# Kernel optimization log

Measured on AMD Instinct MI355X. Metric: run time of the kernel, lower is better.

## Reference

```python
import jax, jax.numpy as jnp
import numpy as np

PI = float(np.pi)


def _layernorm(x, g, b, eps=1e-5):
    mu = jnp.mean(x, axis=-1, keepdims=True)
    var = jnp.var(x, axis=-1, keepdims=True)
    return (x - mu) * jax.lax.rsqrt(var + eps) * g + b


def setup_inputs() -> dict:
    key = jax.random.key(0)
    B, L, D, P = 4, 2048, 256, 32
    ks = jax.random.split(key, 16)

    def lin_w(k, fi, fo):
        return (jax.random.normal(k, (fi, fo), dtype=jnp.float32) / np.sqrt(fi)).astype(jnp.float32)

    inp = {
        'x': jax.random.normal(ks[0], (B, L, D), dtype=jnp.float32),
        'pos_phases': jax.random.normal(ks[1], (L, P), dtype=jnp.float32) * PI,
        'w_mem1v': lin_w(ks[2], D, P), 'b_mem1v': jnp.zeros((P,), jnp.float32),
        'w_mem1o': lin_w(ks[3], P, D), 'b_mem1o': jnp.zeros((D,), jnp.float32),
        'w_off': lin_w(ks[4], D + P, P), 'b_off': jnp.zeros((P,), jnp.float32),
        'w_key': lin_w(ks[5], D, P), 'b_key': jnp.zeros((P,), jnp.float32),
        'w_val': lin_w(ks[6], D, D), 'b_val': jnp.zeros((D,), jnp.float32),
        'w_sk1': lin_w(ks[7], 2 * D, D), 'b_sk1': jnp.zeros((D,), jnp.float32),
        'w_sk2': lin_w(ks[8], D, P), 'b_sk2': jnp.zeros((P,), jnp.float32),
        'w_gate': lin_w(ks[9], D, 1), 'b_gate': jnp.zeros((1,), jnp.float32),
        'ln_g': jnp.ones((D,), jnp.float32), 'ln_b': jnp.zeros((D,), jnp.float32),
        'w_out': lin_w(ks[10], D, D), 'b_out': jnp.zeros((D,), jnp.float32),
    }
    return inp


def reference(x, pos_phases, w_mem1v, b_mem1v, w_mem1o, b_mem1o, w_off, b_off,
              w_key, b_key, w_val, b_val, w_sk1, b_sk1, w_sk2, b_sk2,
              w_gate, b_gate, ln_g, ln_b, w_out, b_out):
    B, L, D = x.shape
    P = pos_phases.shape[-1]

    pos_cos = jnp.cos(pos_phases)  # [L,P]
    pos_sin = jnp.sin(pos_phases)

    # Memory 1: flat [B,L,P] phasor cumulative memory
    v1 = x @ w_mem1v + b_mem1v                       # [B,L,P]
    mem1_cos = jnp.cumsum(pos_cos[None] * v1, axis=1)
    mem1_sin = jnp.cumsum(pos_sin[None] * v1, axis=1)

    offset_input = jnp.concatenate([x, jnp.broadcast_to(pos_phases[None], (B, L, P))], axis=-1)
    offset = jnp.tanh(offset_input @ w_off + b_off) * PI
    oc, os = jnp.cos(offset), jnp.sin(offset)
    query_cos = pos_cos[None] * oc - pos_sin[None] * os
    query_sin = pos_sin[None] * oc + pos_cos[None] * os
    pos_ret = (mem1_cos * query_cos + mem1_sin * query_sin) / np.sqrt(P)
    pos_out = pos_ret @ w_mem1o + b_mem1o            # [B,L,D]

    # Memory 2: full [B,L,P,D] phasor KV cumulative memory
    key_phases = jnp.tanh(x @ w_key + b_key) * PI    # [B,L,P]
    key_cos, key_sin = jnp.cos(key_phases), jnp.sin(key_phases)
    values = x @ w_val + b_val                       # [B,L,D]
    store_gate = jax.nn.sigmoid(x @ w_gate + b_gate) # [B,L,1]

    positions = jnp.arange(1, L + 1, dtype=x.dtype)[None, :, None]
    context_avg = jnp.cumsum(x, axis=1) / positions
    h = jax.nn.gelu(jnp.concatenate([x, context_avg], axis=-1) @ w_sk1 + b_sk1, approximate=False)
    storage_phases = jnp.tanh(h @ w_sk2 + b_sk2) * PI  # [B,L,P]

    gated_v = values * store_gate                    # [B,L,D]
    kv_mem_cos = jnp.cumsum(jnp.cos(storage_phases)[..., None] * gated_v[:, :, None, :], axis=1)  # [B,L,P,D]
    kv_mem_sin = jnp.cumsum(jnp.sin(storage_phases)[..., None] * gated_v[:, :, None, :], axis=1)

    gate_cumsum = jnp.clip(jnp.cumsum(store_gate, axis=1), 1.0, None)  # [B,L,1]
    kv_retrieved = jnp.einsum('blpd,blp->bld', kv_mem_cos, key_cos) + \
                   jnp.einsum('blpd,blp->bld', kv_mem_sin, key_sin)
    kv_retrieved = kv_retrieved / (jnp.sqrt(gate_cumsum) * np.sqrt(P))

    combined = pos_out + kv_retrieved
    return x + _layernorm(combined, ln_g, ln_b) @ w_out + b_out
```

## Files before the change

kernel.cpp:

```cpp
#include <hip/hip_runtime.h>
#include <hip/hip_bf16.h>

constexpr int B_ = 4;
constexpr int L_ = 2048;
constexpr int D_ = 256;
constexpr int P_ = 32;
constexpr int CL = 32;
constexpr int NC = L_ / CL;

#define PI_F 3.14159265358979323846f
#define INV_SQRT_P 0.17677669529663687f

typedef __attribute__((ext_vector_type(8))) short short8_t;
typedef __attribute__((ext_vector_type(4))) float floatx4;

static __device__ inline short f2bf(float f) {
  unsigned int u;
  __builtin_memcpy(&u, &f, 4);
  unsigned int r = (u + 0x7fffu + ((u >> 16) & 1u)) >> 16;
  return (short)r;
}
static __device__ inline float bf2f(short s) {
  unsigned int u = ((unsigned int)(unsigned short)s) << 16;
  float f;
  __builtin_memcpy(&f, &u, 4);
  return f;
}

__global__ void wprep(const float* __restrict__ x, const float* __restrict__ pos,
                      const float* __restrict__ w_val, const float* __restrict__ w_mem1v,
                      const float* __restrict__ w_off, const float* __restrict__ b_off,
                      const float* __restrict__ w_key, const float* __restrict__ w_gate,
                      const float* __restrict__ w_sk1, const float* __restrict__ w_out,
                      const float* __restrict__ w_sk2, const float* __restrict__ w_mem1o,
                      short* __restrict__ WA, short* __restrict__ W1,
                      short* __restrict__ WO, short* __restrict__ W2T,
                      short* __restrict__ W1OT,
                      short* __restrict__ xbf, float* __restrict__ poff) {
  int blk = blockIdx.x, tid = threadIdx.x;
  if (blk < 384) {
    int idx = blk * 256 + tid;
    int n = idx >> 8, k = idx & 255;
    float v;
    if (n < 256) v = w_val[k * 256 + n];
    else if (n < 288) v = w_mem1v[k * 32 + (n - 256)];
    else if (n < 320) v = w_off[k * 32 + (n - 288)];
    else if (n < 352) v = w_key[k * 32 + (n - 320)];
    else if (n == 352) v = w_gate[k];
    else v = 0.f;
    WA[idx] = f2bf(v);
  } else if (blk < 896) {
    int idx = (blk - 384) * 256 + tid;
    int n = idx >> 9, k = idx & 511;
    W1[idx] = f2bf(w_sk1[k * 256 + n]);
  } else if (blk < 1152) {
    int idx = (blk - 896) * 256 + tid;
    int n = idx >> 8, k = idx & 255;
    WO[idx] = f2bf(w_out[k * 256 + n]);
  } else if (blk < 1184) {
    int idx = (blk - 1152) * 256 + tid;
    int p = idx >> 8, k = idx & 255;
    W2T[idx] = f2bf(w_sk2[k * 32 + p]);
  } else if (blk < 1216) {
    int idx = (blk - 1184) * 256 + tid;
    int d = idx >> 5, p = idx & 31;
    W1OT[idx] = f2bf(w_mem1o[p * 256 + d]);
  } else if (blk < 3264) {
    int idx = ((blk - 1216) * 256 + tid) * 4;
    float4 v = *(const float4*)&x[idx];
    short4 o;
    o.x = f2bf(v.x); o.y = f2bf(v.y); o.z = f2bf(v.z); o.w = f2bf(v.w);
    *(short4*)&xbf[idx] = o;
  } else {
    int idx = (blk - 3264) * 256 + tid;
    int l = idx >> 5, p = idx & 31;
    float a = b_off[p];
    for (int j = 0; j < 32; ++j) a += pos[l * 32 + j] * w_off[(256 + j) * 32 + p];
    poff[idx] = a;
  }
}

template <int KTILES, int NBLK, int MODE>
__global__ __launch_bounds__(256) void gemm_k(const short* __restrict__ A0,
                                              const short* __restrict__ A1,
                                              const short* __restrict__ W,
                                              const float* __restrict__ bias,
                                              const float* __restrict__ xres,
                                              float* __restrict__ outf,
                                              short* __restrict__ outb) {
  __shared__ short As[64][136];
  __shared__ short Bs[64][136];
  int tid = threadIdx.x;
  int mg = blockIdx.x / NBLK, ng = blockIdx.x % NBLK;
  int tok0 = mg * 64, n0 = ng * 64;
  int lane = tid & 63, w = tid >> 6;
  int mw = (w & 1) * 32, nw = (w >> 1) * 32;
  floatx4 acc[2][2] = {{{0.f, 0.f, 0.f, 0.f}, {0.f, 0.f, 0.f, 0.f}},
                       {{0.f, 0.f, 0.f, 0.f}, {0.f, 0.f, 0.f, 0.f}}};
  int r2 = tid >> 4, c8 = tid & 15;
  int ml = lane & 15, kq = (lane >> 4) * 8;
  const int K = KTILES * 128;

  for (int kt = 0; kt < KTILES; ++kt) {
    const short* Asrc;
    int cb;
    if (KTILES == 4) {
      Asrc = (kt < 2) ? A0 : A1;
      cb = (kt & 1) * 128;
    } else {
      Asrc = A0;
      cb = kt * 128;
    }
#pragma unroll
    for (int pass = 0; pass < 4; ++pass) {
      int row = pass * 16 + r2;
      *(short8_t*)&As[row][c8 * 8] =
          *(const short8_t*)&Asrc[(tok0 + row) * 256 + cb + c8 * 8];
      *(short8_t*)&Bs[row][c8 * 8] =
          *(const short8_t*)&W[(n0 + row) * K + kt * 128 + c8 * 8];
    }
    __syncthreads();
#pragma unroll
    for (int s = 0; s < 4; ++s) {
      short8_t a0 = *(short8_t*)&As[mw + ml][s * 32 + kq];
      short8_t a1 = *(short8_t*)&As[mw + 16 + ml][s * 32 + kq];
      short8_t b0 = *(short8_t*)&Bs[nw + ml][s * 32 + kq];
      short8_t b1 = *(short8_t*)&Bs[nw + 16 + ml][s * 32 + kq];
      acc[0][0] = __builtin_amdgcn_mfma_f32_16x16x32_bf16(a0, b0, acc[0][0], 0, 0, 0);
      acc[0][1] = __builtin_amdgcn_mfma_f32_16x16x32_bf16(a0, b1, acc[0][1], 0, 0, 0);
      acc[1][0] = __builtin_amdgcn_mfma_f32_16x16x32_bf16(a1, b0, acc[1][0], 0, 0, 0);
      acc[1][1] = __builtin_amdgcn_mfma_f32_16x16x32_bf16(a1, b1, acc[1][1], 0, 0, 0);
    }
    __syncthreads();
  }
  int col = lane & 15, rq = (lane >> 4) * 4;
#pragma unroll
  for (int nt = 0; nt < 2; ++nt) {
    int n = n0 + nw + nt * 16 + col;
    float bv = (MODE == 0) ? 0.f : bias[n];
#pragma unroll
    for (int mt = 0; mt < 2; ++mt) {
#pragma unroll
      for (int rg = 0; rg < 4; ++rg) {
        int tok = tok0 + mw + mt * 16 + rq + rg;
        float v = acc[mt][nt][rg] + bv;
        if (MODE == 0) {
          outb[tok * 384 + n] = f2bf(v);
        } else if (MODE == 1) {
          float g = 0.5f * v * (1.f + erff(v * 0.70710678118654752f));
          outb[tok * 256 + n] = f2bf(g);
        } else {
          outf[tok * 256 + n] = xres[tok * 256 + n] + v;
        }
      }
    }
  }
}

__global__ void kernelA3(const short* __restrict__ Ybf, const float* __restrict__ pos,
                         const float* __restrict__ poff, const float* __restrict__ b_mem1v,
                         const float* __restrict__ b_key, const float* __restrict__ b_gate,
                         const float* __restrict__ b_val,
                         float* __restrict__ m1cT, float* __restrict__ m1sT,
                         float* __restrict__ qc, float* __restrict__ qs,
                         short* __restrict__ K2bf, short* __restrict__ gvT,
                         float* __restrict__ sg) {
  __shared__ float gsh[8];
  int tid = threadIdx.x;
  int tok0 = blockIdx.x * 8;
  int t = tid >> 5, p = tid & 31;
  int tok = tok0 + t, l = tok & (L_ - 1);
  int b = tok >> 11;
  float gate = 1.f / (1.f + expf(-(bf2f(Ybf[tok * 384 + 352]) + b_gate[0])));
  if (p == 0) {
    sg[tok] = gate;
    gsh[t] = gate;
  }
  float v1 = bf2f(Ybf[tok * 384 + 256 + p]) + b_mem1v[p];
  float ph = pos[l * 32 + p];
  float pc = cosf(ph), ps = sinf(ph);
  int idxT = (b * 32 + p) * L_ + l;
  m1cT[idxT] = pc * v1;
  m1sT[idxT] = ps * v1;
  float off = tanhf(bf2f(Ybf[tok * 384 + 288 + p]) + poff[l * 32 + p]) * PI_F;
  float oc = cosf(off), os = sinf(off);
  int idx = tok * 32 + p;
  qc[idx] = pc * oc - ps * os;
  qs[idx] = ps * oc + pc * os;
  float kp = tanhf(bf2f(Ybf[tok * 384 + 320 + p]) + b_key[p]) * PI_F;
  K2bf[tok * 64 + p] = f2bf(cosf(kp));
  K2bf[tok * 64 + 32 + p] = f2bf(sinf(kp));
  __syncthreads();
  {
    int l0 = tok0 & (L_ - 1);
    int bc = (tok0 >> 11) * NC + (l0 >> 5);
    int tl0 = l0 & 31;
    short sv[8];
#pragma unroll
    for (int tt = 0; tt < 8; ++tt)
      sv[tt] = f2bf((bf2f(Ybf[(tok0 + tt) * 384 + tid]) + b_val[tid]) * gsh[tt]);
    *(short8_t*)&gvT[(bc * 256 + tid) * 32 + tl0] = *(short8_t*)sv;
  }
}

__global__ void scan_all(float* __restrict__ m1cT, float* __restrict__ m1sT,
                         float* __restrict__ sg, const float* __restrict__ x,
                         float* __restrict__ ctxsum) {
  int blk = blockIdx.x;
  int tid = threadIdx.x;
  if (blk >= 260) {
    int c2 = blk - 260;
    int b = c2 >> 6, ch = c2 & 63;
    int xb = (b * L_ + ch * 32) * 256 + tid;
    float s = 0.f;
#pragma unroll 8
    for (int i = 0; i < 32; ++i) s += x[xb + i * 256];
    ctxsum[c2 * 256 + tid] = s;
    return;
  }
  int lane = tid & 63, wid = tid >> 6;
  __shared__ float wsum[4];
  float carry = 0.f;
  float* arr;
  int base;
  if (blk < 256) {
    arr = (blk < 128) ? m1cT : m1sT;
    base = (blk & 127) * L_;
  } else {
    arr = sg;
    base = (blk - 256) * L_;
  }
  for (int t0 = 0; t0 < L_; t0 += 256) {
    int l = t0 + tid;
    float v = arr[base + l];
#pragma unroll
    for (int off = 1; off < 64; off <<= 1) {
      float n = __shfl_up(v, off, 64);
      if (lane >= off) v += n;
    }
    if (lane == 63) wsum[wid] = v;
    __syncthreads();
    float add = carry;
    for (int w = 0; w < wid; ++w) add += wsum[w];
    arr[base + l] = v + add;
    carry += wsum[0] + wsum[1] + wsum[2] + wsum[3];
    __syncthreads();
  }
}

__global__ void kernelCtx(const float* __restrict__ x, const float* __restrict__ ctxsum,
                          short* __restrict__ ctxbf) {
  int c2 = blockIdx.x;
  int b = c2 >> 6, ch = c2 & 63;
  int tid = threadIdx.x;
  float run = 0.f;
  int sb = b * 64 * 256 + tid;
  for (int c = 0; c < ch; ++c) run += ctxsum[sb + c * 256];
  int xb = (b * L_ + ch * 32) * 256 + tid;
#pragma unroll 8
  for (int i = 0; i < 32; ++i) {
    run += x[xb + i * 256];
    int l = ch * 32 + i;
    ctxbf[xb + i * 256] = f2bf(run / (float)(l + 1));
  }
}

__global__ __launch_bounds__(256) void kernelCD(const short* __restrict__ hs,
                                                const short* __restrict__ W2T,
                                                const float* __restrict__ b_sk2,
                                                const short* __restrict__ gvT,
                                                short* __restrict__ SPbf,
                                                short* __restrict__ UT) {
  __shared__ __align__(16) short SPL[2][64][40];
  int tid = threadIdx.x;
  int tok0 = blockIdx.x * 64;
  int lane = tid & 63, w = tid >> 6;
  int ml = lane & 15, quad = lane >> 4, kq = quad * 8;
  int m0 = w * 16;
  floatx4 pacc[2] = {};
#pragma unroll
  for (int s = 0; s < 8; ++s) {
    short8_t a = *(const short8_t*)&hs[(tok0 + m0 + ml) * 256 + s * 32 + kq];
    short8_t b0 = *(const short8_t*)&W2T[ml * 256 + s * 32 + kq];
    short8_t b1 = *(const short8_t*)&W2T[(16 + ml) * 256 + s * 32 + kq];
    pacc[0] = __builtin_amdgcn_mfma_f32_16x16x32_bf16(a, b0, pacc[0], 0, 0, 0);
    pacc[1] = __builtin_amdgcn_mfma_f32_16x16x32_bf16(a, b1, pacc[1], 0, 0, 0);
  }
  int cl = w >> 1;
#pragma unroll
  for (int nt = 0; nt < 2; ++nt) {
    int p = nt * 16 + ml;
    float bs = b_sk2[p];
#pragma unroll
    for (int r = 0; r < 4; ++r) {
      int tok = tok0 + m0 + quad * 4 + r;
      float sp = tanhf(pacc[nt][r] + bs) * PI_F;
      short c = f2bf(cosf(sp)), s = f2bf(sinf(sp));
      int tl = (w & 1) * 16 + quad * 4 + r;
      SPL[cl][p][tl] = c;
      SPL[cl][32 + p][tl] = s;
      SPbf[tok * 64 + p] = c;
      SPbf[tok * 64 + 32 + p] = s;
    }
  }
  __syncthreads();
  int c2 = w & 1, dbase = (w >> 1) * 128;
  int bc = blockIdx.x * 2 + c2;
  short8_t a[4];
#pragma unroll
  for (int mt = 0; mt < 4; ++mt) a[mt] = *(short8_t*)&SPL[c2][mt * 16 + ml][kq];
#pragma unroll
  for (int dp = 0; dp < 2; ++dp) {
    floatx4 acc[4][4] = {};
#pragma unroll
    for (int nt = 0; nt < 4; ++nt) {
      short8_t b = *(const short8_t*)&gvT[(bc * 256 + dbase + dp * 64 + nt * 16 + ml) * 32 + kq];
#pragma unroll
      for (int mt = 0; mt < 4; ++mt)
        acc[mt][nt] = __builtin_amdgcn_mfma_f32_16x16x32_bf16(a[mt], b, acc[mt][nt], 0, 0, 0);
    }
#pragma unroll
    for (int mt = 0; mt < 4; ++mt)
#pragma unroll
      for (int nt = 0; nt < 4; ++nt)
#pragma unroll
        for (int r = 0; r < 4; ++r) {
          int q = mt * 16 + quad * 4 + r;
          int d = dbase + dp * 64 + nt * 16 + ml;
          UT[(bc * 256 + d) * 64 + q] = f2bf(acc[mt][nt][r]);
        }
  }
}

__global__ void kernelE(short* __restrict__ UT) {
  int tid = blockIdx.x * 256 + threadIdx.x;
  int q = tid & 63;
  int d = (tid >> 6) & 255;
  int b = tid >> 14;
  int base = ((b * NC) * 256 + d) * 64 + q;
  const int cs = 256 * 64;
  float run = 0.f;
  for (int c0 = 0; c0 < NC; c0 += 8) {
    short v[8];
#pragma unroll
    for (int j = 0; j < 8; ++j) v[j] = UT[base + (c0 + j) * cs];
#pragma unroll
    for (int j = 0; j < 8; ++j) {
      UT[base + (c0 + j) * cs] = f2bf(run);
      run += bf2f(v[j]);
    }
  }
}

__global__ __launch_bounds__(256) void kernelFG(const short* __restrict__ UT,
                                                const short* __restrict__ SPbf,
                                                const short* __restrict__ K2bf,
                                                const short* __restrict__ gvT,
                                                const float* __restrict__ sgc,
                                                const float* __restrict__ m1cT,
                                                const float* __restrict__ m1sT,
                                                const float* __restrict__ qc,
                                                const float* __restrict__ qs,
                                                const short* __restrict__ W1OT,
                                                const float* __restrict__ b_mem1o,
                                                const float* __restrict__ ln_g,
                                                const float* __restrict__ ln_b,
                                                short* __restrict__ cbn) {
  __shared__ __align__(16) short SL[32][40];
  __shared__ __align__(16) short PR[32][40];
  __shared__ float CMB[32][260];
  __shared__ float scl[32], mu_s[32], rs_s[32];
  int tid = threadIdx.x;
  int bc = blockIdx.x;
  int lbase = bc * CL;
  int bb = bc >> 6, lloc = (bc & 63) * 32;
  if (tid < 32) scl[tid] = rsqrtf(fmaxf(sgc[lbase + tid], 1.f)) * INV_SQRT_P;
  for (int it = 0; it < 4; ++it) {
    int i = it * 256 + tid;
    int p = i >> 5, t = i & 31;
    int gT = (bb * 32 + p) * L_ + lloc + t;
    int g = (lbase + t) * 32 + p;
    PR[t][p] = f2bf((m1cT[gT] * qc[g] + m1sT[gT] * qs[g]) * INV_SQRT_P);
  }
  int lane = tid & 63, w = tid >> 6;
  int ml = lane & 15, quad = lane >> 4, kq = quad * 8;
  floatx4 acc[2][4] = {};
  short8_t ka0 = *(const short8_t*)&K2bf[(lbase + ml) * 64 + kq];
  short8_t ka1 = *(const short8_t*)&K2bf[(lbase + 16 + ml) * 64 + kq];
  short8_t kb0 = *(const short8_t*)&K2bf[(lbase + ml) * 64 + 32 + kq];
  short8_t kb1 = *(const short8_t*)&K2bf[(lbase + 16 + ml) * 64 + 32 + kq];
#pragma unroll
  for (int nt = 0; nt < 4; ++nt) {
    short8_t b = *(const short8_t*)&UT[(bc * 256 + w * 64 + nt * 16 + ml) * 64 + kq];
    acc[0][nt] = __builtin_amdgcn_mfma_f32_16x16x32_bf16(ka0, b, acc[0][nt], 0, 0, 0);
    acc[1][nt] = __builtin_amdgcn_mfma_f32_16x16x32_bf16(ka1, b, acc[1][nt], 0, 0, 0);
  }
  if (w == 0) {
    floatx4 sacc[2][2] = {};
#pragma unroll
    for (int ks2 = 0; ks2 < 2; ++ks2) {
      short8_t a0 = (ks2 == 0) ? ka0 : kb0;
      short8_t a1 = (ks2 == 0) ? ka1 : kb1;
      short8_t b0 = *(const short8_t*)&SPbf[(lbase + ml) * 64 + ks2 * 32 + kq];
      short8_t b1 = *(const short8_t*)&SPbf[(lbase + 16 + ml) * 64 + ks2 * 32 + kq];
      sacc[0][0] = __builtin_amdgcn_mfma_f32_16x16x32_bf16(a0, b0, sacc[0][0], 0, 0, 0);
      sacc[0][1] = __builtin_amdgcn_mfma_f32_16x16x32_bf16(a0, b1, sacc[0][1], 0, 0, 0);
      sacc[1][0] = __builtin_amdgcn_mfma_f32_16x16x32_bf16(a1, b0, sacc[1][0], 0, 0, 0);
      sacc[1][1] = __builtin_amdgcn_mfma_f32_16x16x32_bf16(a1, b1, sacc[1][1], 0, 0, 0);
    }
#pragma unroll
    for (int mt = 0; mt < 2; ++mt)
#pragma unroll
      for (int nt = 0; nt < 2; ++nt)
#pragma unroll
        for (int r = 0; r < 4; ++r) {
          int trow = mt * 16 + quad * 4 + r;
          int scol = nt * 16 + ml;
          float v = (scol <= trow) ? sacc[mt][nt][r] : 0.f;
          SL[trow][scol] = f2bf(v);
        }
  }
  __syncthreads();
#pragma unroll
  for (int nt = 0; nt < 4; ++nt) {
    short8_t b = *(const short8_t*)&UT[(bc * 256 + w * 64 + nt * 16 + ml) * 64 + 32 + kq];
    acc[0][nt] = __builtin_amdgcn_mfma_f32_16x16x32_bf16(kb0, b, acc[0][nt], 0, 0, 0);
    acc[1][nt] = __builtin_amdgcn_mfma_f32_16x16x32_bf16(kb1, b, acc[1][nt], 0, 0, 0);
  }
  {
    short8_t a0 = *(short8_t*)&SL[ml][kq];
    short8_t a1 = *(short8_t*)&SL[16 + ml][kq];
#pragma unroll
    for (int nt = 0; nt < 4; ++nt) {
      short8_t b = *(const short8_t*)&gvT[(bc * 256 + w * 64 + nt * 16 + ml) * 32 + kq];
      acc[0][nt] = __builtin_amdgcn_mfma_f32_16x16x32_bf16(a0, b, acc[0][nt], 0, 0, 0);
      acc[1][nt] = __builtin_amdgcn_mfma_f32_16x16x32_bf16(a1, b, acc[1][nt], 0, 0, 0);
    }
  }
  floatx4 macc[2][4] = {};
  {
    short8_t a0 = *(short8_t*)&PR[ml][kq];
    short8_t a1 = *(short8_t*)&PR[16 + ml][kq];
#pragma unroll
    for (int nt = 0; nt < 4; ++nt) {
      short8_t b = *(const short8_t*)&W1OT[(w * 64 + nt * 16 + ml) * 32 + kq];
      macc[0][nt] = __builtin_amdgcn_mfma_f32_16x16x32_bf16(a0, b, macc[0][nt], 0, 0, 0);
      macc[1][nt] = __builtin_amdgcn_mfma_f32_16x16x32_bf16(a1, b, macc[1][nt], 0, 0, 0);
    }
  }
#pragma unroll
  for (int mt = 0; mt < 2; ++mt)
#pragma unroll
    for (int nt = 0; nt < 4; ++nt) {
      int d = w * 64 + nt * 16 + ml;
      float bm = b_mem1o[d];
#pragma unroll
      for (int r = 0; r < 4; ++r) {
        int t = mt * 16 + quad * 4 + r;
        CMB[t][d] = acc[mt][nt][r] * scl[t] + macc[mt][nt][r] + bm;
      }
    }
  __syncthreads();
  {
    int t = tid >> 3, g = tid & 7;
    float s = 0.f, s2 = 0.f;
#pragma unroll
    for (int j = 0; j < 32; ++j) {
      float v = CMB[t][g + j * 8];
      s += v;
      s2 += v * v;
    }
#pragma unroll
    for (int m = 1; m < 8; m <<= 1) {
      s += __shfl_xor(s, m, 64);
      s2 += __shfl_xor(s2, m, 64);
    }
    if (g == 0) {
      float mu = s / (float)D_;
      float var = s2 / (float)D_ - mu * mu;
      mu_s[t] = mu;
      rs_s[t] = rsqrtf(var + 1e-5f);
    }
  }
  __syncthreads();
  {
    float lg = ln_g[tid], lb = ln_b[tid];
#pragma unroll
    for (int t = 0; t < 32; ++t)
      cbn[(lbase + t) * 256 + tid] = f2bf((CMB[t][tid] - mu_s[t]) * rs_s[t] * lg + lb);
  }
}

extern "C" void kernel_launch(void* const* d_in, const int* in_sizes, int n_in,
                              void* d_out, int out_size, void* d_ws, size_t ws_size,
                              hipStream_t stream) {
  const float* x = (const float*)d_in[0];
  const float* pos = (const float*)d_in[1];
  const float* w_mem1v = (const float*)d_in[2];
  const float* b_mem1v = (const float*)d_in[3];
  const float* w_mem1o = (const float*)d_in[4];
  const float* b_mem1o = (const float*)d_in[5];
  const float* w_off = (const float*)d_in[6];
  const float* b_off = (const float*)d_in[7];
  const float* w_key = (const float*)d_in[8];
  const float* b_key = (const float*)d_in[9];
  const float* w_val = (const float*)d_in[10];
  const float* b_val = (const float*)d_in[11];
  const float* w_sk1 = (const float*)d_in[12];
  const float* b_sk1 = (const float*)d_in[13];
  const float* w_sk2 = (const float*)d_in[14];
  const float* b_sk2 = (const float*)d_in[15];
  const float* w_gate = (const float*)d_in[16];
  const float* b_gate = (const float*)d_in[17];
  const float* ln_g = (const float*)d_in[18];
  const float* ln_b = (const float*)d_in[19];
  const float* w_out = (const float*)d_in[20];
  const float* b_out = (const float*)d_in[21];
  float* out = (float*)d_out;
  float* ws = (float*)d_ws;

  const int BLP = B_ * L_ * P_;
  const int BLD = B_ * L_ * D_;
  float* m1cT = ws;
  float* m1sT = m1cT + BLP;
  float* qc = m1sT + BLP;
  float* qs = qc + BLP;
  float* sg = qs + BLP;
  float* poff = sg + B_ * L_;
  float* ctxsum = poff + L_ * P_;
  short* Ybf = (short*)(ctxsum + B_ * 64 * 256);
  short* UT = Ybf;
  short* xbf = UT + (size_t)B_ * NC * 256 * 64;
  short* cbn = xbf;
  short* ctxbf = xbf + BLD;
  short* hs = ctxbf + BLD;
  short* gvT = hs + BLD;
  short* K2bf = gvT + BLD;
  short* SPbf = K2bf + B_ * L_ * 64;
  short* WA = SPbf + B_ * L_ * 64;
  short* W1 = WA + 384 * 256;
  short* WO = W1 + 256 * 512;
  short* W2T = WO + 256 * 256;
  short* W1OT = W2T + 32 * 256;

  wprep<<<3520, 256, 0, stream>>>(x, pos, w_val, w_mem1v, w_off, b_off, w_key, w_gate,
                                  w_sk1, w_out, w_sk2, w_mem1o, WA, W1, WO, W2T, W1OT,
                                  xbf, poff);
  gemm_k<2, 6, 0><<<128 * 6, 256, 0, stream>>>(xbf, nullptr, WA, nullptr, nullptr, nullptr, Ybf);
  kernelA3<<<(B_ * L_) / 8, 256, 0, stream>>>(Ybf, pos, poff, b_mem1v, b_key, b_gate, b_val,
                                              m1cT, m1sT, qc, qs, K2bf, gvT, sg);
  scan_all<<<516, 256, 0, stream>>>(m1cT, m1sT, sg, x, ctxsum);
  kernelCtx<<<256, 256, 0, stream>>>(x, ctxsum, ctxbf);
  gemm_k<4, 4, 1><<<128 * 4, 256, 0, stream>>>(xbf, ctxbf, W1, b_sk1, nullptr, nullptr, hs);
  kernelCD<<<(B_ * L_) / 64, 256, 0, stream>>>(hs, W2T, b_sk2, gvT, SPbf, UT);
  kernelE<<<256, 256, 0, stream>>>(UT);
  kernelFG<<<B_ * NC, 256, 0, stream>>>(UT, SPbf, K2bf, gvT, sg, m1cT, m1sT, qc, qs,
                                        W1OT, b_mem1o, ln_g, ln_b, cbn);
  gemm_k<2, 4, 2><<<128 * 4, 256, 0, stream>>>(cbn, nullptr, WO, b_out, x, out, nullptr);
}
```

Baseline: 190.6 us.

## Fuse GEMMs into consumer kernels and convert weights to bf16 on the fly

Removes the weight/activation prep kernel and the standalone GEMM launches, folding the input projection into the A3 stage, the sk1/sk2 MLP into the CD stage, and the output projection plus residual into the FG stage. Weights are loaded directly from fp32 global memory and rounded to bf16 per fragment, and x is converted inside the GEMM loops. Chunk context sums move into the first kernel. This cuts launches and intermediate round-trips, but adds strided, uncoalesced weight reads repeated in every block and uses only 256 blocks per kernel.

```diff
diff --git a/kernel.cpp b/kernel.cpp
--- a/kernel.cpp
+++ b/kernel.cpp
@@ -27,195 +27,144 @@
   return f;
 }
 
-__global__ void wprep(const float* __restrict__ x, const float* __restrict__ pos,
-                      const float* __restrict__ w_val, const float* __restrict__ w_mem1v,
-                      const float* __restrict__ w_off, const float* __restrict__ b_off,
-                      const float* __restrict__ w_key, const float* __restrict__ w_gate,
-                      const float* __restrict__ w_sk1, const float* __restrict__ w_out,
-                      const float* __restrict__ w_sk2, const float* __restrict__ w_mem1o,
-                      short* __restrict__ WA, short* __restrict__ W1,
-                      short* __restrict__ WO, short* __restrict__ W2T,
-                      short* __restrict__ W1OT,
-                      short* __restrict__ xbf, float* __restrict__ poff) {
-  int blk = blockIdx.x, tid = threadIdx.x;
-  if (blk < 384) {
-    int idx = blk * 256 + tid;
-    int n = idx >> 8, k = idx & 255;
-    float v;
-    if (n < 256) v = w_val[k * 256 + n];
-    else if (n < 288) v = w_mem1v[k * 32 + (n - 256)];
-    else if (n < 320) v = w_off[k * 32 + (n - 288)];
-    else if (n < 352) v = w_key[k * 32 + (n - 320)];
-    else if (n == 352) v = w_gate[k];
-    else v = 0.f;
-    WA[idx] = f2bf(v);
-  } else if (blk < 896) {
-    int idx = (blk - 384) * 256 + tid;
-    int n = idx >> 9, k = idx & 511;
-    W1[idx] = f2bf(w_sk1[k * 256 + n]);
-  } else if (blk < 1152) {
-    int idx = (blk - 896) * 256 + tid;
-    int n = idx >> 8, k = idx & 255;
-    WO[idx] = f2bf(w_out[k * 256 + n]);
-  } else if (blk < 1184) {
-    int idx = (blk - 1152) * 256 + tid;
-    int p = idx >> 8, k = idx & 255;
-    W2T[idx] = f2bf(w_sk2[k * 32 + p]);
-  } else if (blk < 1216) {
-    int idx = (blk - 1184) * 256 + tid;
-    int d = idx >> 5, p = idx & 31;
-    W1OT[idx] = f2bf(w_mem1o[p * 256 + d]);
-  } else if (blk < 3264) {
-    int idx = ((blk - 1216) * 256 + tid) * 4;
-    float4 v = *(const float4*)&x[idx];
-    short4 o;
-    o.x = f2bf(v.x); o.y = f2bf(v.y); o.z = f2bf(v.z); o.w = f2bf(v.w);
-    *(short4*)&xbf[idx] = o;
-  } else {
-    int idx = (blk - 3264) * 256 + tid;
-    int l = idx >> 5, p = idx & 31;
+template <int NCOLS>
+static __device__ inline short8_t loadBfragF32(const float* __restrict__ W,
+                                               int k0, int nloc) {
+  short s[8];
+#pragma unroll
+  for (int j = 0; j < 8; ++j) s[j] = f2bf(W[(k0 + j) * NCOLS + nloc]);
+  return *(short8_t*)s;
+}
+
+static __device__ inline short8_t loadAfragF32(const float* __restrict__ X,
+                                               int row, int k0) {
+  float4 v0 = *(const float4*)&X[row * 256 + k0];
+  float4 v1 = *(const float4*)&X[row * 256 + k0 + 4];
+  short s[8] = {f2bf(v0.x), f2bf(v0.y), f2bf(v0.z), f2bf(v0.w),
+                f2bf(v1.x), f2bf(v1.y), f2bf(v1.z), f2bf(v1.w)};
+  return *(short8_t*)s;
+}
+
+__global__ __launch_bounds__(256) void kernelA3G(
+    const float* __restrict__ x, const float* __restrict__ pos,
+    const float* __restrict__ w_val, const float* __restrict__ w_mem1v,
+    const float* __restrict__ w_off, const float* __restrict__ w_key,
+    const float* __restrict__ w_gate, const float* __restrict__ b_mem1v,
+    const float* __restrict__ b_off, const float* __restrict__ b_key,
+    const float* __restrict__ b_gate, const float* __restrict__ b_val,
+    float* __restrict__ m1cT, float* __restrict__ m1sT,
+    float* __restrict__ qc, float* __restrict__ qs,
+    short* __restrict__ K2bf, short* __restrict__ gvT,
+    float* __restrict__ sg, float* __restrict__ ctxsum) {
+  __shared__ float Yl[32][390];
+  __shared__ float gsh[32];
+  int tid = threadIdx.x;
+  int bc = blockIdx.x;
+  int b = bc >> 6;
+  int lbase = bc * 32;
+  int lane = tid & 63, w = tid >> 6;
+  int ml = lane & 15, quad = lane >> 4, kq = quad * 8;
+
+  floatx4 acc[2][6] = {};
+  const float* xrow = x + (size_t)lbase * 256;
+  for (int ks = 0; ks < 8; ++ks) {
+    int k0 = ks * 32 + kq;
+    short8_t a0 = loadAfragF32(xrow, ml, k0);
+    short8_t a1 = loadAfragF32(xrow, 16 + ml, k0);
+#pragma unroll
+    for (int nt = 0; nt < 6; ++nt) {
+      int n = w * 96 + nt * 16;
+      if (n > 352) continue;
+      short8_t bfr;
+      if (n < 256) bfr = loadBfragF32<256>(w_val, k0, n + ml);
+      else if (n < 288) bfr = loadBfragF32<32>(w_mem1v, k0, n - 256 + ml);
+      else if (n < 320) bfr = loadBfragF32<32>(w_off, k0, n - 288 + ml);
+      else if (n < 352) bfr = loadBfragF32<32>(w_key, k0, n - 320 + ml);
+      else {
+        short s[8];
+#pragma unroll
+        for (int j = 0; j < 8; ++j) s[j] = (ml == 0) ? f2bf(w_gate[k0 + j]) : (short)0;
+        bfr = *(short8_t*)s;
+      }
+      acc[0][nt] = __builtin_amdgcn_mfma_f32_16x16x32_bf16(a0, bfr, acc[0][nt], 0, 0, 0);
+      acc[1][nt] = __builtin_amdgcn_mfma_f32_16x16x32_bf16(a1, bfr, acc[1][nt], 0, 0, 0);
+    }
+  }
+#pragma unroll
+  for (int nt = 0; nt < 6; ++nt) {
+    int n = w * 96 + nt * 16;
+    if (n > 352) continue;
+#pragma unroll
+    for (int mt = 0; mt < 2; ++mt)
+#pragma unroll
+      for (int r = 0; r < 4; ++r)
+        Yl[mt * 16 + quad * 4 + r][n + ml] = acc[mt][nt][r];
+  }
+  __syncthreads();
+
+  for (int h = 0; h < 4; ++h) {
+    int t = h * 8 + (tid >> 5), p = tid & 31;
+    int tok = lbase + t, l = tok & (L_ - 1);
+    float gate = 1.f / (1.f + expf(-(Yl[t][352] + b_gate[0])));
+    if (p == 0) {
+      sg[tok] = gate;
+      gsh[t] = gate;
+    }
+    float v1 = Yl[t][256 + p] + b_mem1v[p];
+    float ph = pos[l * 32 + p];
+    float pc = cosf(ph), ps = sinf(ph);
+    m1cT[(b * 32 + p) * L_ + l] = pc * v1;
+    m1sT[(b * 32 + p) * L_ + l] = ps * v1;
     float a = b_off[p];
     for (int j = 0; j < 32; ++j) a += pos[l * 32 + j] * w_off[(256 + j) * 32 + p];
-    poff[idx] = a;
-  }
-}
-
-template <int KTILES, int NBLK, int MODE>
-__global__ __launch_bounds__(256) void gemm_k(const short* __restrict__ A0,
-                                              const short* __restrict__ A1,
-                                              const short* __restrict__ W,
-                                              const float* __restrict__ bias,
-                                              const float* __restrict__ xres,
-                                              float* __restrict__ outf,
-                                              short* __restrict__ outb) {
-  __shared__ short As[64][136];
-  __shared__ short Bs[64][136];
-  int tid = threadIdx.x;
-  int mg = blockIdx.x / NBLK, ng = blockIdx.x % NBLK;
-  int tok0 = mg * 64, n0 = ng * 64;
-  int lane = tid & 63, w = tid >> 6;
-  int mw = (w & 1) * 32, nw = (w >> 1) * 32;
-  floatx4 acc[2][2] = {{{0.f, 0.f, 0.f, 0.f}, {0.f, 0.f, 0.f, 0.f}},
-                       {{0.f, 0.f, 0.f, 0.f}, {0.f, 0.f, 0.f, 0.f}}};
-  int r2 = tid >> 4, c8 = tid & 15;
-  int ml = lane & 15, kq = (lane >> 4) * 8;
-  const int K = KTILES * 128;
-
-  for (int kt = 0; kt < KTILES; ++kt) {
-    const short* Asrc;
-    int cb;
-    if (KTILES == 4) {
-      Asrc = (kt < 2) ? A0 : A1;
-      cb = (kt & 1) * 128;
-    } else {
-      Asrc = A0;
-      cb = kt * 128;
-    }
-#pragma unroll
-    for (int pass = 0; pass < 4; ++pass) {
-      int row = pass * 16 + r2;
-      *(short8_t*)&As[row][c8 * 8] =
-          *(const short8_t*)&Asrc[(tok0 + row) * 256 + cb + c8 * 8];
-      *(short8_t*)&Bs[row][c8 * 8] =
-          *(const short8_t*)&W[(n0 + row) * K + kt * 128 + c8 * 8];
-    }
-    __syncthreads();
-#pragma unroll
-    for (int s = 0; s < 4; ++s) {
-      short8_t a0 = *(short8_t*)&As[mw + ml][s * 32 + kq];
-      short8_t a1 = *(short8_t*)&As[mw + 16 + ml][s * 32 + kq];
-      short8_t b0 = *(short8_t*)&Bs[nw + ml][s * 32 + kq];
-      short8_t b1 = *(short8_t*)&Bs[nw + 16 + ml][s * 32 + kq];
-      acc[0][0] = __builtin_amdgcn_mfma_f32_16x16x32_bf16(a0, b0, acc[0][0], 0, 0, 0);
-      acc[0][1] = __builtin_amdgcn_mfma_f32_16x16x32_bf16(a0, b1, acc[0][1], 0, 0, 0);
-      acc[1][0] = __builtin_amdgcn_mfma_f32_16x16x32_bf16(a1, b0, acc[1][0], 0, 0, 0);
-      acc[1][1] = __builtin_amdgcn_mfma_f32_16x16x32_bf16(a1, b1, acc[1][1], 0, 0, 0);
-    }
-    __syncthreads();
-  }
-  int col = lane & 15, rq = (lane >> 4) * 4;
-#pragma unroll
-  for (int nt = 0; nt < 2; ++nt) {
-    int n = n0 + nw + nt * 16 + col;
-    float bv = (MODE == 0) ? 0.f : bias[n];
-#pragma unroll
-    for (int mt = 0; mt < 2; ++mt) {
-#pragma unroll
-      for (int rg = 0; rg < 4; ++rg) {
-        int tok = tok0 + mw + mt * 16 + rq + rg;
-        float v = acc[mt][nt][rg] + bv;
-        if (MODE == 0) {
-          outb[tok * 384 + n] = f2bf(v);
-        } else if (MODE == 1) {
-          float g = 0.5f * v * (1.f + erff(v * 0.70710678118654752f));
-          outb[tok * 256 + n] = f2bf(g);
-        } else {
-          outf[tok * 256 + n] = xres[tok * 256 + n] + v;
-        }
-      }
-    }
-  }
-}
-
-__global__ void kernelA3(const short* __restrict__ Ybf, const float* __restrict__ pos,
-                         const float* __restrict__ poff, const float* __restrict__ b_mem1v,
-                         const float* __restrict__ b_key, const float* __restrict__ b_gate,
-                         const float* __restrict__ b_val,
-                         float* __restrict__ m1cT, float* __restrict__ m1sT,
-                         float* __restrict__ qc, float* __restrict__ qs,
-                         short* __restrict__ K2bf, short* __restrict__ gvT,
-                         float* __restrict__ sg) {
-  __shared__ float gsh[8];
-  int tid = threadIdx.x;
-  int tok0 = blockIdx.x * 8;
-  int t = tid >> 5, p = tid & 31;
-  int tok = tok0 + t, l = tok & (L_ - 1);
-  int b = tok >> 11;
-  float gate = 1.f / (1.f + expf(-(bf2f(Ybf[tok * 384 + 352]) + b_gate[0])));
-  if (p == 0) {
-    sg[tok] = gate;
-    gsh[t] = gate;
-  }
-  float v1 = bf2f(Ybf[tok * 384 + 256 + p]) + b_mem1v[p];
-  float ph = pos[l * 32 + p];
-  float pc = cosf(ph), ps = sinf(ph);
-  int idxT = (b * 32 + p) * L_ + l;
-  m1cT[idxT] = pc * v1;
-  m1sT[idxT] = ps * v1;
-  float off = tanhf(bf2f(Ybf[tok * 384 + 288 + p]) + poff[l * 32 + p]) * PI_F;
-  float oc = cosf(off), os = sinf(off);
-  int idx = tok * 32 + p;
-  qc[idx] = pc * oc - ps * os;
-  qs[idx] = ps * oc + pc * os;
-  float kp = tanhf(bf2f(Ybf[tok * 384 + 320 + p]) + b_key[p]) * PI_F;
-  K2bf[tok * 64 + p] = f2bf(cosf(kp));
-  K2bf[tok * 64 + 32 + p] = f2bf(sinf(kp));
-  __syncthreads();
+    float off = tanhf(Yl[t][288 + p] + a) * PI_F;
+    float oc = cosf(off), os = sinf(off);
+    int idx = tok * 32 + p;
+    qc[idx] = pc * oc - ps * os;
+    qs[idx] = ps * oc + pc * os;
+    float kp = tanhf(Yl[t][320 + p] + b_key[p]) * PI_F;
+    K2bf[tok * 64 + p] = f2bf(cosf(kp));
+    K2bf[tok * 64 + 32 + p] = f2bf(sinf(kp));
+  }
+  __syncthreads();
+
   {
-    int l0 = tok0 & (L_ - 1);
-    int bc = (tok0 >> 11) * NC + (l0 >> 5);
-    int tl0 = l0 & 31;
-    short sv[8];
-#pragma unroll
-    for (int tt = 0; tt < 8; ++tt)
-      sv[tt] = f2bf((bf2f(Ybf[(tok0 + tt) * 384 + tid]) + b_val[tid]) * gsh[tt]);
-    *(short8_t*)&gvT[(bc * 256 + tid) * 32 + tl0] = *(short8_t*)sv;
+    int d = tid;
+    float bv = b_val[d];
+    float cs = 0.f;
+    short sv[32];
+#pragma unroll 8
+    for (int t = 0; t < 32; ++t) {
+      cs += x[(size_t)(lbase + t) * 256 + d];
+      sv[t] = f2bf((Yl[t][d] + bv) * gsh[t]);
+    }
+    ctxsum[bc * 256 + d] = cs;
+    int gb = (bc * 256 + d) * 32;
+    *(short8_t*)&gvT[gb] = *(short8_t*)&sv[0];
+    *(short8_t*)&gvT[gb + 8] = *(short8_t*)&sv[8];
+    *(short8_t*)&gvT[gb + 16] = *(short8_t*)&sv[16];
+    *(short8_t*)&gvT[gb + 24] = *(short8_t*)&sv[24];
   }
 }
 
 __global__ void scan_all(float* __restrict__ m1cT, float* __restrict__ m1sT,
                          float* __restrict__ sg, const float* __restrict__ x,
-                         float* __restrict__ ctxsum) {
+                         const float* __restrict__ ctxsum, short* __restrict__ ctxbf) {
   int blk = blockIdx.x;
   int tid = threadIdx.x;
   if (blk >= 260) {
     int c2 = blk - 260;
     int b = c2 >> 6, ch = c2 & 63;
+    float run = 0.f;
+    int sb = b * 64 * 256 + tid;
+    for (int c = 0; c < ch; ++c) run += ctxsum[sb + c * 256];
     int xb = (b * L_ + ch * 32) * 256 + tid;
-    float s = 0.f;
 #pragma unroll 8
-    for (int i = 0; i < 32; ++i) s += x[xb + i * 256];
-    ctxsum[c2 * 256 + tid] = s;
+    for (int i = 0; i < 32; ++i) {
+      run += x[xb + i * 256];
+      int l = ch * 32 + i;
+      ctxbf[xb + i * 256] = f2bf(run / (float)(l + 1));
+    }
     return;
   }
   int lane = tid & 63, wid = tid >> 6;
@@ -248,95 +197,108 @@
   }
 }
 
-__global__ void kernelCtx(const float* __restrict__ x, const float* __restrict__ ctxsum,
-                          short* __restrict__ ctxbf) {
-  int c2 = blockIdx.x;
-  int b = c2 >> 6, ch = c2 & 63;
+__global__ __launch_bounds__(256) void kernelCDg(
+    const float* __restrict__ x, const short* __restrict__ ctxbf,
+    const float* __restrict__ w_sk1, const float* __restrict__ b_sk1,
+    const float* __restrict__ w_sk2, const float* __restrict__ b_sk2,
+    const short* __restrict__ gvT, short* __restrict__ SPbf,
+    short* __restrict__ UT) {
+  __shared__ __align__(16) short hsl[32][264];
+  __shared__ __align__(16) short SPL[64][40];
   int tid = threadIdx.x;
-  float run = 0.f;
-  int sb = b * 64 * 256 + tid;
-  for (int c = 0; c < ch; ++c) run += ctxsum[sb + c * 256];
-  int xb = (b * L_ + ch * 32) * 256 + tid;
-#pragma unroll 8
-  for (int i = 0; i < 32; ++i) {
-    run += x[xb + i * 256];
-    int l = ch * 32 + i;
-    ctxbf[xb + i * 256] = f2bf(run / (float)(l + 1));
-  }
-}
-
-__global__ __launch_bounds__(256) void kernelCD(const short* __restrict__ hs,
-                                                const short* __restrict__ W2T,
-                                                const float* __restrict__ b_sk2,
-                                                const short* __restrict__ gvT,
-                                                short* __restrict__ SPbf,
-                                                short* __restrict__ UT) {
-  __shared__ __align__(16) short SPL[2][64][40];
-  int tid = threadIdx.x;
-  int tok0 = blockIdx.x * 64;
+  int bc = blockIdx.x;
+  int lbase = bc * 32;
   int lane = tid & 63, w = tid >> 6;
   int ml = lane & 15, quad = lane >> 4, kq = quad * 8;
-  int m0 = w * 16;
-  floatx4 pacc[2] = {};
-#pragma unroll
-  for (int s = 0; s < 8; ++s) {
-    short8_t a = *(const short8_t*)&hs[(tok0 + m0 + ml) * 256 + s * 32 + kq];
-    short8_t b0 = *(const short8_t*)&W2T[ml * 256 + s * 32 + kq];
-    short8_t b1 = *(const short8_t*)&W2T[(16 + ml) * 256 + s * 32 + kq];
-    pacc[0] = __builtin_amdgcn_mfma_f32_16x16x32_bf16(a, b0, pacc[0], 0, 0, 0);
-    pacc[1] = __builtin_amdgcn_mfma_f32_16x16x32_bf16(a, b1, pacc[1], 0, 0, 0);
-  }
-  int cl = w >> 1;
-#pragma unroll
-  for (int nt = 0; nt < 2; ++nt) {
-    int p = nt * 16 + ml;
+
+  floatx4 acc[2][4] = {};
+  const float* xrow = x + (size_t)lbase * 256;
+  for (int ks = 0; ks < 16; ++ks) {
+    int k0 = ks * 32 + kq;
+    short8_t a0, a1;
+    if (ks < 8) {
+      a0 = loadAfragF32(xrow, ml, k0);
+      a1 = loadAfragF32(xrow, 16 + ml, k0);
+    } else {
+      a0 = *(const short8_t*)&ctxbf[(size_t)(lbase + ml) * 256 + (k0 - 256)];
+      a1 = *(const short8_t*)&ctxbf[(size_t)(lbase + 16 + ml) * 256 + (k0 - 256)];
+    }
+#pragma unroll
+    for (int nt = 0; nt < 4; ++nt) {
+      short8_t bfr = loadBfragF32<256>(w_sk1, k0, w * 64 + nt * 16 + ml);
+      acc[0][nt] = __builtin_amdgcn_mfma_f32_16x16x32_bf16(a0, bfr, acc[0][nt], 0, 0, 0);
+      acc[1][nt] = __builtin_amdgcn_mfma_f32_16x16x32_bf16(a1, bfr, acc[1][nt], 0, 0, 0);
+    }
+  }
+#pragma unroll
+  for (int nt = 0; nt < 4; ++nt) {
+    int n = w * 64 + nt * 16 + ml;
+    float bs = b_sk1[n];
+#pragma unroll
+    for (int mt = 0; mt < 2; ++mt)
+#pragma unroll
+      for (int r = 0; r < 4; ++r) {
+        float v = acc[mt][nt][r] + bs;
+        float g = 0.5f * v * (1.f + erff(v * 0.70710678118654752f));
+        hsl[mt * 16 + quad * 4 + r][n] = f2bf(g);
+      }
+  }
+  __syncthreads();
+
+  {
+    int m0 = (w & 1) * 16, n0 = (w >> 1) * 16;
+    floatx4 pacc = {};
+#pragma unroll
+    for (int ks = 0; ks < 8; ++ks) {
+      int k0 = ks * 32 + kq;
+      short8_t a = *(short8_t*)&hsl[m0 + ml][k0];
+      short8_t bfr = loadBfragF32<32>(w_sk2, k0, n0 + ml);
+      pacc = __builtin_amdgcn_mfma_f32_16x16x32_bf16(a, bfr, pacc, 0, 0, 0);
+    }
+    int p = n0 + ml;
     float bs = b_sk2[p];
 #pragma unroll
     for (int r = 0; r < 4; ++r) {
-      int tok = tok0 + m0 + quad * 4 + r;
-      float sp = tanhf(pacc[nt][r] + bs) * PI_F;
+      int tl = m0 + quad * 4 + r;
+      int tok = lbase + tl;
+      float sp = tanhf(pacc[r] + bs) * PI_F;
       short c = f2bf(cosf(sp)), s = f2bf(sinf(sp));
-      int tl = (w & 1) * 16 + quad * 4 + r;
-      SPL[cl][p][tl] = c;
-      SPL[cl][32 + p][tl] = s;
+      SPL[p][tl] = c;
+      SPL[32 + p][tl] = s;
       SPbf[tok * 64 + p] = c;
       SPbf[tok * 64 + 32 + p] = s;
     }
   }
   __syncthreads();
-  int c2 = w & 1, dbase = (w >> 1) * 128;
-  int bc = blockIdx.x * 2 + c2;
+
   short8_t a[4];
 #pragma unroll
-  for (int mt = 0; mt < 4; ++mt) a[mt] = *(short8_t*)&SPL[c2][mt * 16 + ml][kq];
-#pragma unroll
-  for (int dp = 0; dp < 2; ++dp) {
-    floatx4 acc[4][4] = {};
-#pragma unroll
-    for (int nt = 0; nt < 4; ++nt) {
-      short8_t b = *(const short8_t*)&gvT[(bc * 256 + dbase + dp * 64 + nt * 16 + ml) * 32 + kq];
-#pragma unroll
-      for (int mt = 0; mt < 4; ++mt)
-        acc[mt][nt] = __builtin_amdgcn_mfma_f32_16x16x32_bf16(a[mt], b, acc[mt][nt], 0, 0, 0);
-    }
+  for (int mt = 0; mt < 4; ++mt) a[mt] = *(short8_t*)&SPL[mt * 16 + ml][kq];
+  floatx4 uacc[4][4] = {};
+#pragma unroll
+  for (int nt = 0; nt < 4; ++nt) {
+    short8_t bfr = *(const short8_t*)&gvT[(bc * 256 + w * 64 + nt * 16 + ml) * 32 + kq];
 #pragma unroll
     for (int mt = 0; mt < 4; ++mt)
-#pragma unroll
-      for (int nt = 0; nt < 4; ++nt)
-#pragma unroll
-        for (int r = 0; r < 4; ++r) {
-          int q = mt * 16 + quad * 4 + r;
-          int d = dbase + dp * 64 + nt * 16 + ml;
-          UT[(bc * 256 + d) * 64 + q] = f2bf(acc[mt][nt][r]);
-        }
-  }
+      uacc[mt][nt] = __builtin_amdgcn_mfma_f32_16x16x32_bf16(a[mt], bfr, uacc[mt][nt], 0, 0, 0);
+  }
+#pragma unroll
+  for (int mt = 0; mt < 4; ++mt)
+#pragma unroll
+    for (int nt = 0; nt < 4; ++nt)
+#pragma unroll
+      for (int r = 0; r < 4; ++r) {
+        int q = mt * 16 + quad * 4 + r;
+        int d = w * 64 + nt * 16 + ml;
+        UT[(bc * 256 + d) * 64 + q] = f2bf(uacc[mt][nt][r]);
+      }
 }
 
 __global__ void kernelE(short* __restrict__ UT) {
-  int tid = blockIdx.x * 256 + threadIdx.x;
-  int q = tid & 63;
-  int d = (tid >> 6) & 255;
-  int b = tid >> 14;
+  int gt = blockIdx.x * 256 + threadIdx.x;
+  int q = gt & 63;
+  int d = (gt >> 6) & 255;
+  int b = gt >> 14;
   int base = ((b * NC) * 256 + d) * 64 + q;
   const int cs = 256 * 64;
   float run = 0.f;
@@ -352,28 +314,27 @@
   }
 }
 
-__global__ __launch_bounds__(256) void kernelFG(const short* __restrict__ UT,
-                                                const short* __restrict__ SPbf,
-                                                const short* __restrict__ K2bf,
-                                                const short* __restrict__ gvT,
-                                                const float* __restrict__ sgc,
-                                                const float* __restrict__ m1cT,
-                                                const float* __restrict__ m1sT,
-                                                const float* __restrict__ qc,
-                                                const float* __restrict__ qs,
-                                                const short* __restrict__ W1OT,
-                                                const float* __restrict__ b_mem1o,
-                                                const float* __restrict__ ln_g,
-                                                const float* __restrict__ ln_b,
-                                                short* __restrict__ cbn) {
+__global__ __launch_bounds__(256) void kernelFGO(
+    const short* __restrict__ UT, const short* __restrict__ SPbf,
+    const short* __restrict__ K2bf, const short* __restrict__ gvT,
+    const float* __restrict__ sgc, const float* __restrict__ m1cT,
+    const float* __restrict__ m1sT, const float* __restrict__ qc,
+    const float* __restrict__ qs, const float* __restrict__ w_mem1o,
+    const float* __restrict__ b_mem1o, const float* __restrict__ ln_g,
+    const float* __restrict__ ln_b, const float* __restrict__ x,
+    const float* __restrict__ w_out, const float* __restrict__ b_out,
+    float* __restrict__ out) {
   __shared__ __align__(16) short SL[32][40];
   __shared__ __align__(16) short PR[32][40];
   __shared__ float CMB[32][260];
+  __shared__ __align__(16) short CBN[32][264];
   __shared__ float scl[32], mu_s[32], rs_s[32];
   int tid = threadIdx.x;
   int bc = blockIdx.x;
   int lbase = bc * CL;
   int bb = bc >> 6, lloc = (bc & 63) * 32;
+  int lane = tid & 63, w = tid >> 6;
+  int ml = lane & 15, quad = lane >> 4, kq = quad * 8;
   if (tid < 32) scl[tid] = rsqrtf(fmaxf(sgc[lbase + tid], 1.f)) * INV_SQRT_P;
   for (int it = 0; it < 4; ++it) {
     int i = it * 256 + tid;
@@ -382,8 +343,6 @@
     int g = (lbase + t) * 32 + p;
     PR[t][p] = f2bf((m1cT[gT] * qc[g] + m1sT[gT] * qs[g]) * INV_SQRT_P);
   }
-  int lane = tid & 63, w = tid >> 6;
-  int ml = lane & 15, quad = lane >> 4, kq = quad * 8;
   floatx4 acc[2][4] = {};
   short8_t ka0 = *(const short8_t*)&K2bf[(lbase + ml) * 64 + kq];
   short8_t ka1 = *(const short8_t*)&K2bf[(lbase + 16 + ml) * 64 + kq];
@@ -443,7 +402,7 @@
     short8_t a1 = *(short8_t*)&PR[16 + ml][kq];
 #pragma unroll
     for (int nt = 0; nt < 4; ++nt) {
-      short8_t b = *(const short8_t*)&W1OT[(w * 64 + nt * 16 + ml) * 32 + kq];
+      short8_t b = loadBfragF32<256>(w_mem1o, kq, w * 64 + nt * 16 + ml);
       macc[0][nt] = __builtin_amdgcn_mfma_f32_16x16x32_bf16(a0, b, macc[0][nt], 0, 0, 0);
       macc[1][nt] = __builtin_amdgcn_mfma_f32_16x16x32_bf16(a1, b, macc[1][nt], 0, 0, 0);
     }
@@ -487,7 +446,32 @@
     float lg = ln_g[tid], lb = ln_b[tid];
 #pragma unroll
     for (int t = 0; t < 32; ++t)
-      cbn[(lbase + t) * 256 + tid] = f2bf((CMB[t][tid] - mu_s[t]) * rs_s[t] * lg + lb);
+      CBN[t][tid] = f2bf((CMB[t][tid] - mu_s[t]) * rs_s[t] * lg + lb);
+  }
+  __syncthreads();
+  floatx4 oacc[2][4] = {};
+  for (int ks = 0; ks < 8; ++ks) {
+    int k0 = ks * 32 + kq;
+    short8_t a0 = *(short8_t*)&CBN[ml][k0];
+    short8_t a1 = *(short8_t*)&CBN[16 + ml][k0];
+#pragma unroll
+    for (int nt = 0; nt < 4; ++nt) {
+      short8_t b = loadBfragF32<256>(w_out, k0, w * 64 + nt * 16 + ml);
+      oacc[0][nt] = __builtin_amdgcn_mfma_f32_16x16x32_bf16(a0, b, oacc[0][nt], 0, 0, 0);
+      oacc[1][nt] = __builtin_amdgcn_mfma_f32_16x16x32_bf16(a1, b, oacc[1][nt], 0, 0, 0);
+    }
+  }
+#pragma unroll
+  for (int nt = 0; nt < 4; ++nt) {
+    int n = w * 64 + nt * 16 + ml;
+    float bo = b_out[n];
+#pragma unroll
+    for (int mt = 0; mt < 2; ++mt)
+#pragma unroll
+      for (int r = 0; r < 4; ++r) {
+        int tok = lbase + mt * 16 + quad * 4 + r;
+        out[(size_t)tok * 256 + n] = x[(size_t)tok * 256 + n] + oacc[mt][nt][r] + bo;
+      }
   }
 }
 
@@ -526,35 +510,21 @@
   float* qc = m1sT + BLP;
   float* qs = qc + BLP;
   float* sg = qs + BLP;
-  float* poff = sg + B_ * L_;
-  float* ctxsum = poff + L_ * P_;
-  short* Ybf = (short*)(ctxsum + B_ * 64 * 256);
-  short* UT = Ybf;
-  short* xbf = UT + (size_t)B_ * NC * 256 * 64;
-  short* cbn = xbf;
-  short* ctxbf = xbf + BLD;
-  short* hs = ctxbf + BLD;
-  short* gvT = hs + BLD;
+  float* ctxsum = sg + B_ * L_;
+  short* ctxbf = (short*)(ctxsum + B_ * 64 * 256);
+  short* gvT = ctxbf + BLD;
   short* K2bf = gvT + BLD;
   short* SPbf = K2bf + B_ * L_ * 64;
-  short* WA = SPbf + B_ * L_ * 64;
-  short* W1 = WA + 384 * 256;
-  short* WO = W1 + 256 * 512;
-  short* W2T = WO + 256 * 256;
-  short* W1OT = W2T + 32 * 256;
-
-  wprep<<<3520, 256, 0, stream>>>(x, pos, w_val, w_mem1v, w_off, b_off, w_key, w_gate,
-                                  w_sk1, w_out, w_sk2, w_mem1o, WA, W1, WO, W2T, W1OT,
-                                  xbf, poff);
-  gemm_k<2, 6, 0><<<128 * 6, 256, 0, stream>>>(xbf, nullptr, WA, nullptr, nullptr, nullptr, Ybf);
-  kernelA3<<<(B_ * L_) / 8, 256, 0, stream>>>(Ybf, pos, poff, b_mem1v, b_key, b_gate, b_val,
-                                              m1cT, m1sT, qc, qs, K2bf, gvT, sg);
-  scan_all<<<516, 256, 0, stream>>>(m1cT, m1sT, sg, x, ctxsum);
-  kernelCtx<<<256, 256, 0, stream>>>(x, ctxsum, ctxbf);
-  gemm_k<4, 4, 1><<<128 * 4, 256, 0, stream>>>(xbf, ctxbf, W1, b_sk1, nullptr, nullptr, hs);
-  kernelCD<<<(B_ * L_) / 64, 256, 0, stream>>>(hs, W2T, b_sk2, gvT, SPbf, UT);
+  short* UT = SPbf + B_ * L_ * 64;
+
+  kernelA3G<<<256, 256, 0, stream>>>(x, pos, w_val, w_mem1v, w_off, w_key, w_gate,
+                                     b_mem1v, b_off, b_key, b_gate, b_val,
+                                     m1cT, m1sT, qc, qs, K2bf, gvT, sg, ctxsum);
+  scan_all<<<516, 256, 0, stream>>>(m1cT, m1sT, sg, x, ctxsum, ctxbf);
+  kernelCDg<<<256, 256, 0, stream>>>(x, ctxbf, w_sk1, b_sk1, w_sk2, b_sk2, gvT,
+                                     SPbf, UT);
   kernelE<<<256, 256, 0, stream>>>(UT);
-  kernelFG<<<B_ * NC, 256, 0, stream>>>(UT, SPbf, K2bf, gvT, sg, m1cT, m1sT, qc, qs,
-                                        W1OT, b_mem1o, ln_g, ln_b, cbn);
-  gemm_k<2, 4, 2><<<128 * 4, 256, 0, stream>>>(cbn, nullptr, WO, b_out, x, out, nullptr);
-}
+  kernelFGO<<<256, 256, 0, stream>>>(UT, SPbf, K2bf, gvT, sg, m1cT, m1sT, qc, qs,
+                                     w_mem1o, b_mem1o, ln_g, ln_b, x, w_out, b_out,
+                                     out);
+}
```

Measured after the change: 208.4 us. 9.3% more time.
